# Kernel optimization log

Hardware: AMD Instinct MI355X
Metric: run time of the kernel (lower is better)

The kernel has to match this reference:

```python
import jax, jax.numpy as jnp
import numpy as np

B, N, D = 64, 197, 768
H, E, R = 12, 8, 8


def setup_inputs() -> dict:
    key = jax.random.key(0)
    ks = jax.random.split(key, 8)
    s = 0.02
    return {
        "tokens": jax.random.normal(ks[0], (B, N, D), dtype=jnp.float32),
        "qkv_w": jax.random.normal(ks[1], (3 * D, D), dtype=jnp.float32) * s,
        "qkv_b": jax.random.normal(ks[2], (3 * D,), dtype=jnp.float32) * s,
        "proj_w": jax.random.normal(ks[3], (D, D), dtype=jnp.float32) * s,
        "proj_b": jax.random.normal(ks[4], (D,), dtype=jnp.float32) * s,
        "gate_w": jax.random.normal(ks[5], (E, D), dtype=jnp.float32) * s,
        "lora_a": jax.random.normal(ks[6], (E, D, R), dtype=jnp.float32) * s,
        "lora_b": jax.random.normal(ks[7], (E, R, 3 * D), dtype=jnp.float32) * s,
    }


def reference(tokens, qkv_w, qkv_b, proj_w, proj_b, gate_w, lora_a, lora_b):
    b, n, d = tokens.shape
    hd = d // H
    scale = hd ** (-0.5)
    # frozen qkv projection: [b, n, 3d]
    qkv = jnp.einsum("bnd,kd->bnk", tokens, qkv_w) + qkv_b
    # LoRA-MoE delta (soft router over experts)
    gates = jax.nn.softmax(jnp.einsum("bnd,ed->bne", tokens, gate_w), axis=-1)
    h = jnp.einsum("bnd,edr->bner", tokens, lora_a)  # [b,n,E,R]
    delta = jnp.einsum("bner,erk,bne->bnk", h, lora_b, gates)  # [b,n,3d]
    # adding delta before the reshape is identical to per-q/k/v addition after
    qkv = (qkv + delta).reshape(b, n, 3, H, hd).transpose(2, 0, 3, 1, 4)
    q, k, v = qkv[0], qkv[1], qkv[2]  # each [b,H,n,hd]
    attn = jax.nn.softmax(jnp.einsum("bhqd,bhkd->bhqk", q, k) * scale, axis=-1)
    out = jnp.einsum("bhqk,bhkd->bhqd", attn, v)
    out = out.transpose(0, 2, 1, 3).reshape(b, n, d)
    return jnp.einsum("bnd,kd->bnk", out, proj_w) + proj_b
```

## Files before the change

kernel.cpp:

```cpp
#include <hip/hip_runtime.h>
#include <hip/hip_bf16.h>

typedef __hip_bfloat16 BF16;
typedef __attribute__((ext_vector_type(8))) short bf16x8;
typedef __attribute__((ext_vector_type(4))) float f32x4;
typedef __attribute__((ext_vector_type(4))) int int4v;

#define MTOK 12608
#define D_IN 768
#define KAUG 832
#define N_QKV 2304

#define AS1 __attribute__((address_space(1)))
#define AS3 __attribute__((address_space(3)))
#define SB0() __builtin_amdgcn_sched_barrier(0)

__global__ __launch_bounds__(256) void prep_waug_k(const float* __restrict__ qkv_w,
                                                   const float* __restrict__ lora_b,
                                                   BF16* __restrict__ Waug) {
  int idx = blockIdx.x*256 + threadIdx.x;
  if (idx >= N_QKV*KAUG) return;
  int k = idx / KAUG, c = idx - k*KAUG;
  float v = (c < D_IN) ? qkv_w[k*D_IN + c] : lora_b[(size_t)(c - D_IN)*N_QKV + k];
  Waug[idx] = (BF16)v;
}

__global__ __launch_bounds__(256) void prep_pb_k(const float* __restrict__ proj_w,
                                                 BF16* __restrict__ Pb) {
  int idx = blockIdx.x*256 + threadIdx.x;
  if (idx < D_IN*D_IN) Pb[idx] = (BF16)proj_w[idx];
}

__global__ __launch_bounds__(256) void prep_lat_k(const float* __restrict__ lora_a,
                                                  BF16* __restrict__ LAt) {
  int idx = blockIdx.x*256 + threadIdx.x;
  if (idx >= 64*D_IN) return;
  int j = idx / D_IN, d = idx - j*D_IN;
  LAt[idx] = (BF16)lora_a[(size_t)(j >> 3)*6144 + d*8 + (j & 7)];
}

__global__ __launch_bounds__(256) void token_prep_k(const float* __restrict__ tokens,
                                                    const float* __restrict__ gate_w,
                                                    BF16* __restrict__ Aaug,
                                                    float* __restrict__ gates) {
  int w = blockIdx.x*4 + (threadIdx.x >> 6);
  int lane = threadIdx.x & 63;
  if (w >= MTOK) return;
  const float* x = tokens + (size_t)w*D_IN;
  float xv[12];
  #pragma unroll
  for (int i=0;i<12;++i) xv[i] = x[lane + 64*i];
  #pragma unroll
  for (int i=0;i<12;++i) Aaug[(size_t)w*KAUG + lane + 64*i] = (BF16)xv[i];
  float g[8] = {0,0,0,0,0,0,0,0};
  #pragma unroll
  for (int i=0;i<12;++i) {
    int d = lane + 64*i;
    #pragma unroll
    for (int e=0;e<8;++e) g[e] += xv[i]*gate_w[e*D_IN + d];
  }
  #pragma unroll
  for (int e=0;e<8;++e) {
    #pragma unroll
    for (int off=32; off; off >>= 1) g[e] += __shfl_xor(g[e], off);
  }
  float mx = g[0];
  #pragma unroll
  for (int e=1;e<8;++e) mx = fmaxf(mx, g[e]);
  float pe[8]; float ssum = 0.f;
  #pragma unroll
  for (int e=0;e<8;++e) { pe[e] = __expf(g[e]-mx); ssum += pe[e]; }
  float inv = 1.f/ssum;
  if (lane < 8) {
    float val = 0.f;
    #pragma unroll
    for (int e=0;e<8;++e) val = (lane==e) ? pe[e]*inv : val;
    gates[(size_t)w*8 + lane] = val;
  }
}

template<int ROWS>
__device__ __forceinline__ void stage_bt(const BF16* __restrict__ g, int ldg, int row0, int M,
                                         BF16* lds, int kbase, int t) {
  constexpr int NIT = ROWS*8/256;
  #pragma unroll
  for (int it=0; it<NIT; ++it) {
    int c = it*256 + t;
    int r = c >> 3, kc = c & 7;
    int rg = row0 + r;
    rg = (rg < M) ? rg : (M-1);
    const BF16* gp = g + (size_t)rg*ldg + kbase + kc*8;
    BF16* lp = lds + (it*256 + (t & ~63))*8;
    __builtin_amdgcn_global_load_lds((const AS1 void*)gp, (AS3 void*)lp, 16, 0, 0);
  }
}

template<int BM, int BN, int EPI>
__global__ __launch_bounds__(256,3) void gemm_bt_k(const BF16* __restrict__ A, int lda,
                                                   const BF16* __restrict__ Bt, int ldb,
                                                   const float* __restrict__ aux,
                                                   void* __restrict__ Cv, int ldc,
                                                   int M, int K) {
  constexpr int BK = 64;
  constexpr int WM = BM/2, WN = BN/2;
  constexpr int MF = WM/16, NF = WN/16;
  __shared__ BF16 Al[BM*BK];
  __shared__ BF16 Bl[BN*BK];
  const int n0 = blockIdx.x*BN, m0 = blockIdx.y*BM;
  const int t = threadIdx.x, lane = t & 63, wid = t >> 6;
  const int wm = (wid >> 1)*WM, wn = (wid & 1)*WN;
  f32x4 acc[MF][NF] = {};
  const int KT = K/BK;
  for (int kt=0; kt<KT; ++kt) {
    stage_bt<BM>(A, lda, m0, M, Al, kt*BK, t);
    stage_bt<BN>(Bt, ldb, n0, 1<<30, Bl, kt*BK, t);
    __syncthreads();
    #pragma unroll
    for (int kk=0; kk<2; ++kk) {
      bf16x8 a[MF], b[NF];
      const int col = kk*32 + (lane >> 4)*8;
      #pragma unroll
      for (int m=0;m<MF;++m) a[m] = *(const bf16x8*)(Al + (wm + m*16 + (lane & 15))*BK + col);
      #pragma unroll
      for (int n=0;n<NF;++n) b[n] = *(const bf16x8*)(Bl + (wn + n*16 + (lane & 15))*BK + col);
      #pragma unroll
      for (int m=0;m<MF;++m)
        #pragma unroll
        for (int n=0;n<NF;++n)
          acc[m][n] = __builtin_amdgcn_mfma_f32_16x16x32_bf16(a[m], b[n], acc[m][n], 0, 0, 0);
    }
    __syncthreads();
  }
  #pragma unroll
  for (int m=0;m<MF;++m) {
    #pragma unroll
    for (int n=0;n<NF;++n) {
      const int rb = m0 + wm + m*16 + (lane >> 4)*4;
      const int c = n0 + wn + n*16 + (lane & 15);
      #pragma unroll
      for (int j=0;j<4;++j) {
        const int r = rb + j;
        if (r < M) {
          float v = acc[m][n][j];
          if (EPI == 0) {
            v *= aux[(size_t)r*8 + (c >> 3)];
            ((BF16*)Cv)[(size_t)r*ldc + c] = (BF16)v;
          } else if (EPI == 1) {
            v += aux[c];
            ((BF16*)Cv)[(size_t)r*ldc + c] = (BF16)v;
          } else {
            v += aux[c];
            ((float*)Cv)[(size_t)r*ldc + c] = v;
          }
        }
      }
    }
  }
}

template<int EPI, int NBN, int LDA, int LDB, int LDC>
__global__ __launch_bounds__(256,2) void gemm2_k(const BF16* __restrict__ A,
                                                 const BF16* __restrict__ Bt,
                                                 const float* __restrict__ bias,
                                                 void* __restrict__ Cv,
                                                 int M, int K) {
  __shared__ BF16 Lsh[2][2][8192];
  const int t = threadIdx.x, lane = t & 63, wid = t >> 6;
  const int nwg = gridDim.x;
  const int q8 = nwg >> 3, r8 = nwg & 7;
  const int xcd = blockIdx.x & 7, pos = blockIdx.x >> 3;
  const int wg = (xcd < r8 ? xcd*(q8+1) : r8*(q8+1) + (xcd - r8)*q8) + pos;
  const int mb = wg / NBN, nb = wg - mb*NBN;
  const int m0 = mb*128, n0 = nb*128;
  const int KT = K/64;
  const int q4 = lane & 15;
  const int wm = (wid >> 1)*64, wn = (wid & 1)*64;

  const BF16 *sA[4], *sB[4];
  #pragma unroll
  for (int it=0; it<4; ++it) {
    int c = it*256 + t;
    int r = c >> 3, p = c & 7;
    int sc = p ^ (r & 7);
    int ra = m0 + r; ra = ra < M ? ra : M-1;
    sA[it] = A  + (size_t)ra*LDA + sc*8;
    sB[it] = Bt + (size_t)(n0 + r)*LDB + sc*8;
  }
  auto stageAB = [&](int buf, int tile) {
    #pragma unroll
    for (int it=0; it<4; ++it)
      __builtin_amdgcn_global_load_lds((const AS1 void*)(sA[it] + tile*64),
        (AS3 void*)(&Lsh[buf][0][0] + (it*256 + (t & ~63))*8), 16, 0, 0);
    #pragma unroll
    for (int it=0; it<4; ++it)
      __builtin_amdgcn_global_load_lds((const AS1 void*)(sB[it] + tile*64),
        (AS3 void*)(&Lsh[buf][1][0] + (it*256 + (t & ~63))*8), 16, 0, 0);
  };

  const int sw = (q4 & 7) << 3;
  const int ck[2] = { (((lane >> 4)*8)) ^ sw, ((32 + (lane >> 4)*8)) ^ sw };

  f32x4 acc[4][4] = {};
  stageAB(0, 0);
  asm volatile("s_waitcnt vmcnt(0)" ::: "memory"); SB0();
  __builtin_amdgcn_s_barrier();

  for (int kt = 0; kt < KT; ++kt) {
    const int buf = kt & 1;
    if (kt+1 < KT) stageAB(buf^1, kt+1);
    bf16x8 a[4][2], b[4][2];
    #pragma unroll
    for (int m=0;m<4;++m)
      #pragma unroll
      for (int kk=0;kk<2;++kk)
        a[m][kk] = *(const bf16x8*)(&Lsh[buf][0][0] + (wm + m*16 + q4)*64 + ck[kk]);
    #pragma unroll
    for (int n=0;n<4;++n)
      #pragma unroll
      for (int kk=0;kk<2;++kk)
        b[n][kk] = *(const bf16x8*)(&Lsh[buf][1][0] + (wn + n*16 + q4)*64 + ck[kk]);
    asm volatile("s_waitcnt lgkmcnt(0)" ::: "memory"); SB0();
    __builtin_amdgcn_s_setprio(1);
    #pragma unroll
    for (int kk=0;kk<2;++kk)
      #pragma unroll
      for (int m=0;m<4;++m)
        #pragma unroll
        for (int n=0;n<4;++n)
          acc[m][n] = __builtin_amdgcn_mfma_f32_16x16x32_bf16(a[m][kk], b[n][kk], acc[m][n], 0,0,0);
    __builtin_amdgcn_s_setprio(0);
    SB0();
    if (kt+1 < KT) asm volatile("s_waitcnt vmcnt(0)" ::: "memory");
    SB0();
    __builtin_amdgcn_s_barrier();
  }

  float bv[4];
  #pragma unroll
  for (int n=0;n<4;++n) bv[n] = bias[n0 + wn + n*16 + q4];
  #pragma unroll
  for (int m=0;m<4;++m) {
    #pragma unroll
    for (int j=0;j<4;++j) {
      const int r = m0 + wm + m*16 + (lane >> 4)*4 + j;
      if (r < M) {
        #pragma unroll
        for (int n=0;n<4;++n) {
          float v = acc[m][n][j] + bv[n];
          const size_t idx = (size_t)r*LDC + n0 + wn + n*16 + q4;
          if (EPI == 1) ((BF16*)Cv)[idx] = (BF16)v;
          else          ((float*)Cv)[idx] = v;
        }
      }
    }
  }
}

__global__ __launch_bounds__(256,2) void attn_k(const BF16* __restrict__ QKV,
                                                BF16* __restrict__ O) {
  constexpr int KSTR = 72;
  constexpr int VSTR = 232;
  constexpr int PSTR = 40;
  __shared__ BF16 Kl[208*KSTR];
  __shared__ BF16 Vt[64*VSTR];
  __shared__ BF16 Pl[4][16*PSTR];
  const int bh = blockIdx.x;
  const int b = bh / 12, h = bh - b*12;
  const size_t rowbase = (size_t)b*197;
  const int t = threadIdx.x, lane = t & 63, wid = t >> 6;
  const BF16 z = (BF16)0.0f;
  for (int c = t; c < 208*8; c += 256) {
    int r = c >> 3, kc = c & 7;
    int4v val = {0,0,0,0};
    if (r < 197) val = *(const int4v*)(QKV + (rowbase + r)*N_QKV + 768 + h*64 + kc*8);
    *(int4v*)(Kl + r*KSTR + kc*8) = val;
  }
  for (int c = t; c < 208*8; c += 256) {
    int r = c >> 3, kc = c & 7;
    if (r < 197) {
      int4v val = *(const int4v*)(QKV + (rowbase + r)*N_QKV + 1536 + h*64 + kc*8);
      const BF16* pv = (const BF16*)&val;
      #pragma unroll
      for (int i=0;i<8;++i) Vt[(kc*8 + i)*VSTR + r] = pv[i];
    } else {
      #pragma unroll
      for (int i=0;i<8;++i) Vt[(kc*8 + i)*VSTR + r] = z;
    }
  }
  for (int c = t; c < 64*24; c += 256) {
    int d = c / 24, k2 = 208 + (c - d*24);
    Vt[d*VSTR + k2] = z;
  }
  __syncthreads();

  for (int chunk = wid; chunk < 13; chunk += 4) {
    const int q0 = chunk*16;
    int qr = q0 + (lane & 15);
    qr = (qr < 197) ? qr : 196;
    bf16x8 qa[2];
    #pragma unroll
    for (int kk=0;kk<2;++kk)
      qa[kk] = *(const bf16x8*)(QKV + (rowbase + qr)*N_QKV + h*64 + kk*32 + (lane >> 4)*8);
    f32x4 zf = {0.f,0.f,0.f,0.f};
    f32x4 s[14];
    #pragma unroll
    for (int nf=0;nf<14;++nf) s[nf] = zf;
    #pragma unroll
    for (int nf=0;nf<13;++nf) {
      #pragma unroll
      for (int kk=0;kk<2;++kk) {
        bf16x8 kb = *(const bf16x8*)(Kl + (nf*16 + (lane & 15))*KSTR + kk*32 + (lane >> 4)*8);
        s[nf] = __builtin_amdgcn_mfma_f32_16x16x32_bf16(qa[kk], kb, s[nf], 0, 0, 0);
      }
    }
    float mrow[4] = {-1e30f,-1e30f,-1e30f,-1e30f};
    float lrow[4] = {0.f,0.f,0.f,0.f};
    #pragma unroll
    for (int nf=0;nf<13;++nf) {
      const int cg = nf*16 + (lane & 15);
      #pragma unroll
      for (int j=0;j<4;++j) {
        float v = s[nf][j]*0.125f;
        v = (cg < 197) ? v : -1e30f;
        s[nf][j] = v;
        mrow[j] = fmaxf(mrow[j], v);
      }
    }
    #pragma unroll
    for (int j=0;j<4;++j) {
      #pragma unroll
      for (int off=1; off<16; off<<=1) mrow[j] = fmaxf(mrow[j], __shfl_xor(mrow[j], off));
    }
    #pragma unroll
    for (int nf=0;nf<13;++nf) {
      #pragma unroll
      for (int j=0;j<4;++j) {
        float p = __expf(s[nf][j] - mrow[j]);
        s[nf][j] = p;
        lrow[j] += p;
      }
    }
    #pragma unroll
    for (int j=0;j<4;++j) {
      #pragma unroll
      for (int off=1; off<16; off<<=1) lrow[j] += __shfl_xor(lrow[j], off);
    }
    BF16* P = &Pl[wid][0];
    f32x4 o[4] = {};
    #pragma unroll
    for (int kc=0; kc<7; ++kc) {
      asm volatile("s_waitcnt lgkmcnt(0)" ::: "memory");
      __builtin_amdgcn_sched_barrier(0);
      #pragma unroll
      for (int half=0; half<2; ++half) {
        const int nf = kc*2 + half;
        #pragma unroll
        for (int j=0;j<4;++j)
          P[((lane >> 4)*4 + j)*PSTR + half*16 + (lane & 15)] = (BF16)s[nf][j];
      }
      asm volatile("s_waitcnt lgkmcnt(0)" ::: "memory");
      __builtin_amdgcn_sched_barrier(0);
      bf16x8 pa = *(const bf16x8*)(P + (lane & 15)*PSTR + (lane >> 4)*8);
      #pragma unroll
      for (int df=0; df<4; ++df) {
        bf16x8 vb = *(const bf16x8*)(Vt + (df*16 + (lane & 15))*VSTR + kc*32 + (lane >> 4)*8);
        o[df] = __builtin_amdgcn_mfma_f32_16x16x32_bf16(pa, vb, o[df], 0, 0, 0);
      }
    }
    #pragma unroll
    for (int df=0; df<4; ++df) {
      #pragma unroll
      for (int j=0;j<4;++j) {
        const int r = q0 + (lane >> 4)*4 + j;
        if (r < 197) {
          float val = o[df][j] / lrow[j];
          O[(rowbase + r)*768 + h*64 + df*16 + (lane & 15)] = (BF16)val;
        }
      }
    }
  }
}

extern "C" void kernel_launch(void* const* d_in, const int* in_sizes, int n_in,
                              void* d_out, int out_size, void* d_ws, size_t ws_size,
                              hipStream_t stream) {
  const float* tokens = (const float*)d_in[0];
  const float* qkv_w  = (const float*)d_in[1];
  const float* qkv_b  = (const float*)d_in[2];
  const float* proj_w = (const float*)d_in[3];
  const float* proj_b = (const float*)d_in[4];
  const float* gate_w = (const float*)d_in[5];
  const float* lora_a = (const float*)d_in[6];
  const float* lora_b = (const float*)d_in[7];

  size_t off = 0;
  auto take = [&](size_t bytes) {
    off = (off + 255) & ~(size_t)255;
    void* p = (char*)d_ws + off;
    off += bytes;
    return p;
  };
  BF16* Waug  = (BF16*)take((size_t)N_QKV*KAUG*2);
  BF16* Pb    = (BF16*)take((size_t)D_IN*D_IN*2);
  BF16* LAt   = (BF16*)take((size_t)64*D_IN*2);
  BF16* Aaug  = (BF16*)take((size_t)MTOK*KAUG*2);
  float* gates= (float*)take((size_t)MTOK*8*4);
  BF16* QKVb  = (BF16*)take((size_t)MTOK*N_QKV*2);
  BF16* Oc    = (BF16*)take((size_t)MTOK*D_IN*2);

  prep_waug_k<<<(N_QKV*KAUG + 255)/256, 256, 0, stream>>>(qkv_w, lora_b, Waug);
  prep_pb_k<<<(D_IN*D_IN + 255)/256, 256, 0, stream>>>(proj_w, Pb);
  prep_lat_k<<<(64*D_IN + 255)/256, 256, 0, stream>>>(lora_a, LAt);
  token_prep_k<<<MTOK/4, 256, 0, stream>>>(tokens, gate_w, Aaug, gates);
  gemm_bt_k<64,64,0><<<dim3(1, MTOK/64), 256, 0, stream>>>(
      Aaug, KAUG, LAt, D_IN, gates, (void*)(Aaug + 768), KAUG, MTOK, D_IN);
  gemm2_k<1, 18, KAUG, KAUG, N_QKV><<<99*18, 256, 0, stream>>>(
      Aaug, Waug, qkv_b, (void*)QKVb, MTOK, KAUG);
  attn_k<<<768, 256, 0, stream>>>(QKVb, Oc);
  gemm2_k<2, 6, D_IN, D_IN, D_IN><<<99*6, 256, 0, stream>>>(
      Oc, Pb, proj_b, d_out, MTOK, D_IN);
}
```

Before: 178.8 us.

## Compute transposed S tile and move P to registers via cross-lane shuffles

Swaps the MFMA operand order so each lane holds the scores of one query row across four keys. Row max and row sum then need only two cross-lane shuffles instead of four per row with a 16-lane butterfly. The probabilities are packed to bf16 pairs and rearranged into the PV A-operand with ds_bpermute shuffles. This removes the per-wave LDS staging buffer and its waitcnt barriers, at the cost of more shuffle and select instructions in the PV loop.

After: 195.6 us. +9.4%, slower.

```diff
diff --git a/kernel.cpp b/kernel.cpp
--- a/kernel.cpp
+++ b/kernel.cpp
@@ -256,14 +256,18 @@
   }
 }
 
+__device__ __forceinline__ int pack2bf(float lo, float hi) {
+  BF16 a = (BF16)lo, b = (BF16)hi;
+  unsigned short al = *(unsigned short*)&a, bh = *(unsigned short*)&b;
+  return (int)(((unsigned)bh << 16) | (unsigned)al);
+}
+
 __global__ __launch_bounds__(256,2) void attn_k(const BF16* __restrict__ QKV,
                                                 BF16* __restrict__ O) {
   constexpr int KSTR = 72;
   constexpr int VSTR = 232;
-  constexpr int PSTR = 40;
   __shared__ BF16 Kl[208*KSTR];
   __shared__ BF16 Vt[64*VSTR];
-  __shared__ BF16 Pl[4][16*PSTR];
   const int bh = blockIdx.x;
   const int b = bh / 12, h = bh - b*12;
   const size_t rowbase = (size_t)b*197;
@@ -293,88 +297,95 @@
   }
   __syncthreads();
 
+  const int g = lane >> 4;
+  const int q4 = lane & 15;
+
   for (int chunk = wid; chunk < 13; chunk += 4) {
     const int q0 = chunk*16;
-    int qr = q0 + (lane & 15);
+    int qr = q0 + q4;
     qr = (qr < 197) ? qr : 196;
     bf16x8 qa[2];
     #pragma unroll
     for (int kk=0;kk<2;++kk)
-      qa[kk] = *(const bf16x8*)(QKV + (rowbase + qr)*N_QKV + h*64 + kk*32 + (lane >> 4)*8);
+      qa[kk] = *(const bf16x8*)(QKV + (rowbase + qr)*N_QKV + h*64 + kk*32 + g*8);
     f32x4 zf = {0.f,0.f,0.f,0.f};
-    f32x4 s[14];
-    #pragma unroll
-    for (int nf=0;nf<14;++nf) s[nf] = zf;
+    f32x4 s[13];
+    #pragma unroll
+    for (int nf=0;nf<13;++nf) s[nf] = zf;
     #pragma unroll
     for (int nf=0;nf<13;++nf) {
       #pragma unroll
       for (int kk=0;kk<2;++kk) {
-        bf16x8 kb = *(const bf16x8*)(Kl + (nf*16 + (lane & 15))*KSTR + kk*32 + (lane >> 4)*8);
-        s[nf] = __builtin_amdgcn_mfma_f32_16x16x32_bf16(qa[kk], kb, s[nf], 0, 0, 0);
-      }
-    }
-    float mrow[4] = {-1e30f,-1e30f,-1e30f,-1e30f};
-    float lrow[4] = {0.f,0.f,0.f,0.f};
+        bf16x8 kb = *(const bf16x8*)(Kl + (nf*16 + q4)*KSTR + kk*32 + g*8);
+        s[nf] = __builtin_amdgcn_mfma_f32_16x16x32_bf16(kb, qa[kk], s[nf], 0, 0, 0);
+      }
+    }
+    float m = -1e30f;
     #pragma unroll
     for (int nf=0;nf<13;++nf) {
-      const int cg = nf*16 + (lane & 15);
       #pragma unroll
       for (int j=0;j<4;++j) {
+        const int kg = nf*16 + g*4 + j;
         float v = s[nf][j]*0.125f;
-        v = (cg < 197) ? v : -1e30f;
+        v = (kg < 197) ? v : -1e30f;
         s[nf][j] = v;
-        mrow[j] = fmaxf(mrow[j], v);
-      }
-    }
-    #pragma unroll
-    for (int j=0;j<4;++j) {
-      #pragma unroll
-      for (int off=1; off<16; off<<=1) mrow[j] = fmaxf(mrow[j], __shfl_xor(mrow[j], off));
-    }
+        m = fmaxf(m, v);
+      }
+    }
+    m = fmaxf(m, __shfl_xor(m, 16));
+    m = fmaxf(m, __shfl_xor(m, 32));
+    float lsum = 0.f;
     #pragma unroll
     for (int nf=0;nf<13;++nf) {
       #pragma unroll
       for (int j=0;j<4;++j) {
-        float p = __expf(s[nf][j] - mrow[j]);
+        float p = __expf(s[nf][j] - m);
         s[nf][j] = p;
-        lrow[j] += p;
-      }
-    }
-    #pragma unroll
-    for (int j=0;j<4;++j) {
-      #pragma unroll
-      for (int off=1; off<16; off<<=1) lrow[j] += __shfl_xor(lrow[j], off);
-    }
-    BF16* P = &Pl[wid][0];
+        lsum += p;
+      }
+    }
+    lsum += __shfl_xor(lsum, 16);
+    lsum += __shfl_xor(lsum, 32);
+    int pk[14][2];
+    #pragma unroll
+    for (int nf=0;nf<13;++nf) {
+      pk[nf][0] = pack2bf(s[nf][0], s[nf][1]);
+      pk[nf][1] = pack2bf(s[nf][2], s[nf][3]);
+    }
+    pk[13][0] = 0; pk[13][1] = 0;
+    const int src1 = q4 + ((g & 1) << 5);
+    const int src2 = src1 + 16;
+    const bool hi = (g >> 1) != 0;
     f32x4 o[4] = {};
     #pragma unroll
     for (int kc=0; kc<7; ++kc) {
-      asm volatile("s_waitcnt lgkmcnt(0)" ::: "memory");
-      __builtin_amdgcn_sched_barrier(0);
-      #pragma unroll
-      for (int half=0; half<2; ++half) {
-        const int nf = kc*2 + half;
-        #pragma unroll
-        for (int j=0;j<4;++j)
-          P[((lane >> 4)*4 + j)*PSTR + half*16 + (lane & 15)] = (BF16)s[nf][j];
-      }
-      asm volatile("s_waitcnt lgkmcnt(0)" ::: "memory");
-      __builtin_amdgcn_sched_barrier(0);
-      bf16x8 pa = *(const bf16x8*)(P + (lane & 15)*PSTR + (lane >> 4)*8);
+      int a0 = __shfl(pk[2*kc][0], src1),   b0 = __shfl(pk[2*kc+1][0], src1);
+      int a1 = __shfl(pk[2*kc][1], src1),   b1 = __shfl(pk[2*kc+1][1], src1);
+      int a2 = __shfl(pk[2*kc][0], src2),   b2 = __shfl(pk[2*kc+1][0], src2);
+      int a3 = __shfl(pk[2*kc][1], src2),   b3 = __shfl(pk[2*kc+1][1], src2);
+      int4v w;
+      w[0] = hi ? b0 : a0;
+      w[1] = hi ? b1 : a1;
+      w[2] = hi ? b2 : a2;
+      w[3] = hi ? b3 : a3;
+      bf16x8 pa = *(bf16x8*)&w;
       #pragma unroll
       for (int df=0; df<4; ++df) {
-        bf16x8 vb = *(const bf16x8*)(Vt + (df*16 + (lane & 15))*VSTR + kc*32 + (lane >> 4)*8);
+        bf16x8 vb = *(const bf16x8*)(Vt + (df*16 + q4)*VSTR + kc*32 + g*8);
         o[df] = __builtin_amdgcn_mfma_f32_16x16x32_bf16(pa, vb, o[df], 0, 0, 0);
       }
     }
+    float ldiv[4];
+    #pragma unroll
+    for (int j=0;j<4;++j) ldiv[j] = __shfl(lsum, g*4 + j);
     #pragma unroll
     for (int df=0; df<4; ++df) {
       #pragma unroll
       for (int j=0;j<4;++j) {
-        const int r = q0 + (lane >> 4)*4 + j;
+        const int r = q0 + g*4 + j;
         if (r < 197) {
-          float val = o[df][j] / lrow[j];
-          O[(rowbase + r)*768 + h*64 + df*16 + (lane & 15)] = (BF16)val;
+          float val = o[df][j] / ldiv[j];
+          O[(rowbase + r)*768 + h*64 + df*16 + q4] = (BF16)val;
         }
       }
     }
```
